# Performance work log

Measured on AMD Instinct MI355X. Metric: run time of the kernel, lower is better.

The kernel has to match this reference:

```python
import jax, jax.numpy as jnp
import numpy as np

B, H, L, N = 128, 1024, 256, 64  # batch, d_model, seq len (l_max), SSM state size


def setup_inputs() -> dict:
    key = jax.random.key(0)
    ks = jax.random.split(key, 8)
    x = jax.random.normal(ks[0], (B, H, L), dtype=jnp.float32)
    # S4D init: dt log-uniform in [1e-3, 1e-1], A = -1/2 + i*pi*n, C ~ N(0,1)
    log_dt = jnp.log(10.0 ** jax.random.uniform(ks[1], (H,), minval=-3.0, maxval=-1.0)).astype(jnp.float32)
    A_real_log = jnp.log(0.5 * jnp.ones((H, N), dtype=jnp.float32))
    A_imag = jnp.tile(jnp.pi * jnp.arange(N, dtype=jnp.float32), (H, 1))
    C_re = jax.random.normal(ks[2], (H, N), dtype=jnp.float32)
    C_im = jax.random.normal(ks[3], (H, N), dtype=jnp.float32)
    D = jax.random.normal(ks[4], (H,), dtype=jnp.float32)
    W_out = (jax.random.normal(ks[5], (2 * H, H), dtype=jnp.float32) / np.sqrt(H)).astype(jnp.float32)
    b_out = jnp.zeros((2 * H,), dtype=jnp.float32)
    return dict(x=x, log_dt=log_dt, A_real_log=A_real_log, A_imag=A_imag,
                C_re=C_re, C_im=C_im, D=D, W_out=W_out, b_out=b_out)


def _s4d_kernel(log_dt, A_real_log, A_imag, C_re, C_im, length):
    """S4D convolution kernel (ZOH discretization), shape (H, length)."""
    dt = jnp.exp(log_dt)[:, None]                      # (H, 1)
    A = -jnp.exp(A_real_log) + 1j * A_imag             # (H, N) complex
    C = C_re + 1j * C_im                               # (H, N)
    dtA = A * dt                                       # (H, N)
    C_disc = C * (jnp.exp(dtA) - 1.0) / A              # ZOH-discretized C
    t = jnp.arange(length, dtype=jnp.float32)
    K = jnp.exp(dtA[:, :, None] * t)                   # (H, N, L) Vandermonde
    return 2.0 * jnp.einsum('hn,hnl->hl', C_disc, K).real


def reference(x, log_dt, A_real_log, A_imag, C_re, C_im, D, W_out, b_out):
    Bq, Hq, Lq = x.shape
    k = _s4d_kernel(log_dt, A_real_log, A_imag, C_re, C_im, Lq)  # (H, L)
    n_fft = 2 * Lq
    k_f = jnp.fft.rfft(k, n=n_fft)                     # (H, L+1)
    x_f = jnp.fft.rfft(x, n=n_fft, axis=-1)            # (B, H, L+1)
    y = jnp.fft.irfft(x_f * k_f[None], n=n_fft, axis=-1)[..., :Lq]
    y = y + D[None, :, None] * x                       # skip connection
    y = jax.nn.gelu(y)                                 # FFTConv activation
    # output linear (d_model -> 2*d_model) + GLU over channel dim
    y = jnp.einsum('bhl,gh->bgl', y, W_out) + b_out[None, :, None]
    a, b = jnp.split(y, 2, axis=1)
    return a * jax.nn.sigmoid(b)                       # (B, H, L)
```

## Files before the change

kernel.cpp:

```cpp
#include <hip/hip_runtime.h>
#include <hip/hip_bf16.h>
#include <cstdint>
#include <cstddef>

typedef __bf16 bf16x8 __attribute__((ext_vector_type(8)));
typedef float  f32x4  __attribute__((ext_vector_type(4)));
typedef unsigned short u16x8 __attribute__((ext_vector_type(8)));

__device__ __forceinline__ unsigned short f2bf(float f) {
    unsigned u = __builtin_bit_cast(unsigned, f);
    u += 0x7fffu + ((u >> 16) & 1u);
    return (unsigned short)(u >> 16);
}
__device__ __forceinline__ float bf2f(unsigned short u) {
    unsigned v = ((unsigned)u) << 16;
    return __builtin_bit_cast(float, v);
}
__device__ __forceinline__ float gelu_tanh(float x) {
    float z = 0.7978845608028654f * (x + 0.044715f * x * x * x);
    float e = __expf(2.0f * z);
    float t = 1.0f - 2.0f / (e + 1.0f);
    return 0.5f * x * (1.0f + t);
}

__global__ void k_build(const float* __restrict__ log_dt,
                        const float* __restrict__ arl,
                        const float* __restrict__ aim,
                        const float* __restrict__ cre,
                        const float* __restrict__ cim,
                        const float* __restrict__ Dp,
                        unsigned short* __restrict__ Tg) {
    __shared__ float sRe[64], sIm[64], sCr[64], sCi[64];
    __shared__ float kk[256];
    const int h = blockIdx.x;
    const int t = threadIdx.x;
    if (t < 64) {
        float dt  = expf(log_dt[h]);
        float ar  = -expf(arl[h * 64 + t]);
        float ai  = aim[h * 64 + t];
        float dre = ar * dt, dim = ai * dt;
        float er  = expf(dre);
        float s, c;
        sincosf(dim, &s, &c);
        float em1r = er * c - 1.0f, em1i = er * s;
        float cr = cre[h * 64 + t], ci = cim[h * 64 + t];
        float pr = cr * em1r - ci * em1i;
        float pi = cr * em1i + ci * em1r;
        float inv = 1.0f / (ar * ar + ai * ai);
        sCr[t] = (pr * ar + pi * ai) * inv;
        sCi[t] = (pi * ar - pr * ai) * inv;
        sRe[t] = dre; sIm[t] = dim;
    }
    __syncthreads();
    float acc = 0.0f;
    const float tf = (float)t;
    #pragma unroll 8
    for (int n = 0; n < 64; n++) {
        float er = expf(sRe[n] * tf);
        float s, c;
        sincosf(sIm[n] * tf, &s, &c);
        acc += sCr[n] * er * c - sCi[n] * er * s;
    }
    kk[t] = 2.0f * acc;
    __syncthreads();
    const float Dh = Dp[h];
    unsigned short* dst = Tg + (size_t)h * 16384;
    for (int c = t; c < 1024; c += 256) {
        const int d = c >> 6, q4 = (c >> 4) & 3, mm = c & 15;
        u16x8 hv, lv;
        #pragma unroll
        for (int e = 0; e < 8; e++) {
            const int idx = 16 * d + mm - (q4 * 8 + e);
            float v = (idx >= 0) ? kk[idx] : 0.0f;
            if (idx == 0) v += Dh;
            unsigned short hb = f2bf(v);
            hv[e] = hb;
            lv[e] = f2bf(v - bf2f(hb));
        }
        *(u16x8*)(dst + c * 8)        = hv;
        *(u16x8*)(dst + 8192 + c * 8) = lv;
    }
}

__global__ __launch_bounds__(256, 2)
void conv_mfma(const float* __restrict__ x,
               const unsigned short* __restrict__ Tg,
               unsigned short* __restrict__ yt2) {
    __shared__ __align__(16) unsigned short smem[32768];
    const int h = blockIdx.x, tid = threadIdx.x;
    const int w = tid >> 6, lane = tid & 63, m = lane & 15, q4 = lane >> 4;

    {
        const unsigned short* tg = Tg + (size_t)h * 16384;
        #pragma unroll
        for (int i = 0; i < 8; i++) {
            int q = i * 256 + tid;
            __builtin_amdgcn_global_load_lds(
                (const __attribute__((address_space(1))) void*)(tg + q * 8),
                (__attribute__((address_space(3))) void*)(smem + q * 8), 16, 0, 0);
        }
    }

    const int sb = tid >> 1, half = tid & 1;
    const float* xrow = x + ((size_t)(sb * 1024 + h) << 8);

    float4 cur[8], nxt[8];
    #pragma unroll
    for (int s = 0; s < 8; s++) cur[s] = *(const float4*)(xrow + half * 32 + s * 4);

    auto STAGE_X = [&](int tile) {
        unsigned short* Xn = smem + 16384 + (tile & 1) * 8192;
        #pragma unroll
        for (int s = 0; s < 8; s++) {
            float4 v = cur[s];
            ushort4 hv, lv;
            hv.x = f2bf(v.x); lv.x = f2bf(v.x - bf2f(hv.x));
            hv.y = f2bf(v.y); lv.y = f2bf(v.y - bf2f(hv.y));
            hv.z = f2bf(v.z); lv.z = f2bf(v.z - bf2f(hv.z));
            hv.w = f2bf(v.w); lv.w = f2bf(v.w - bf2f(hv.w));
            const int base = (((s >> 1) * 128 + sb) << 3) + (s & 1) * 4;
            *(ushort4*)(Xn + base)        = hv;
            *(ushort4*)(Xn + 4096 + base) = lv;
        }
    };

    if (half == 0) STAGE_X(0);

    f32x4 acc[8][4];
    #pragma unroll
    for (int a = 0; a < 8; a++)
        #pragma unroll
        for (int b = 0; b < 4; b++) acc[a][b] = (f32x4){0.f, 0.f, 0.f, 0.f};

    __syncthreads();

    const int fi = (q4 * 16 + m) * 8;

    auto MFMA_BODY = [&](int jt) {
        const unsigned short* Xb = smem + 16384 + (jt & 1) * 8192;
        const int j2 = jt << 1;
        const bool a0 = (w      >= j2);
        const bool a1 = (w + 4  >= j2);
        const bool a2 = (w + 8  >= j2);
        const bool a3 = (w + 12 >= j2);
        bf16x8 th0, tl0, th1, tl1, th2, tl2, th3, tl3;
        if (a0) { int d = w      - j2; th0 = *(const bf16x8*)(smem + d * 512 + fi); tl0 = *(const bf16x8*)(smem + 8192 + d * 512 + fi); }
        if (a1) { int d = w + 4  - j2; th1 = *(const bf16x8*)(smem + d * 512 + fi); tl1 = *(const bf16x8*)(smem + 8192 + d * 512 + fi); }
        if (a2) { int d = w + 8  - j2; th2 = *(const bf16x8*)(smem + d * 512 + fi); tl2 = *(const bf16x8*)(smem + 8192 + d * 512 + fi); }
        if (a3) { int d = w + 12 - j2; th3 = *(const bf16x8*)(smem + d * 512 + fi); tl3 = *(const bf16x8*)(smem + 8192 + d * 512 + fi); }
        #pragma unroll
        for (int fb = 0; fb < 8; fb++) {
            const int xo = (q4 * 128 + fb * 16 + m) * 8;
            bf16x8 xh = *(const bf16x8*)(Xb + xo);
            bf16x8 xl = *(const bf16x8*)(Xb + 4096 + xo);
            if (a0) { acc[fb][0] = __builtin_amdgcn_mfma_f32_16x16x32_bf16(xh, th0, acc[fb][0], 0, 0, 0);
                      acc[fb][0] = __builtin_amdgcn_mfma_f32_16x16x32_bf16(xl, th0, acc[fb][0], 0, 0, 0);
                      acc[fb][0] = __builtin_amdgcn_mfma_f32_16x16x32_bf16(xh, tl0, acc[fb][0], 0, 0, 0); }
            if (a1) { acc[fb][1] = __builtin_amdgcn_mfma_f32_16x16x32_bf16(xh, th1, acc[fb][1], 0, 0, 0);
                      acc[fb][1] = __builtin_amdgcn_mfma_f32_16x16x32_bf16(xl, th1, acc[fb][1], 0, 0, 0);
                      acc[fb][1] = __builtin_amdgcn_mfma_f32_16x16x32_bf16(xh, tl1, acc[fb][1], 0, 0, 0); }
            if (a2) { acc[fb][2] = __builtin_amdgcn_mfma_f32_16x16x32_bf16(xh, th2, acc[fb][2], 0, 0, 0);
                      acc[fb][2] = __builtin_amdgcn_mfma_f32_16x16x32_bf16(xl, th2, acc[fb][2], 0, 0, 0);
                      acc[fb][2] = __builtin_amdgcn_mfma_f32_16x16x32_bf16(xh, tl2, acc[fb][2], 0, 0, 0); }
            if (a3) { acc[fb][3] = __builtin_amdgcn_mfma_f32_16x16x32_bf16(xh, th3, acc[fb][3], 0, 0, 0);
                      acc[fb][3] = __builtin_amdgcn_mfma_f32_16x16x32_bf16(xl, th3, acc[fb][3], 0, 0, 0);
                      acc[fb][3] = __builtin_amdgcn_mfma_f32_16x16x32_bf16(xh, tl3, acc[fb][3], 0, 0, 0); }
        }
    };

    #pragma unroll 1
    for (int g = 0; g < 4; g++) {
        if (g < 3) {
            #pragma unroll
            for (int s = 0; s < 8; s++)
                nxt[s] = *(const float4*)(xrow + (g + 1) * 64 + half * 32 + s * 4);
        }
        MFMA_BODY(2 * g);
        if (half == 1) STAGE_X(2 * g + 1);
        __syncthreads();
        MFMA_BODY(2 * g + 1);
        if (g < 3) {
            #pragma unroll
            for (int s = 0; s < 8; s++) cur[s] = nxt[s];
            if (half == 0) STAGE_X(2 * g + 2);
        }
        __syncthreads();
    }

    const size_t ybase = (size_t)h * 32768;
    #pragma unroll
    for (int p = 0; p < 2; p++) {
        #pragma unroll
        for (int tt = 0; tt < 2; tt++) {
            const int ti = p * 2 + tt;
            const int lr = (w + 4 * ti) * 16 + m - p * 128;
            #pragma unroll
            for (int fb = 0; fb < 8; fb++) {
                #pragma unroll
                for (int rg = 0; rg < 4; rg++) {
                    const int b = fb * 16 + q4 * 4 + rg;
                    smem[b * 136 + lr] = f2bf(gelu_tanh(acc[fb][ti][rg]));
                }
            }
        }
        __syncthreads();
        #pragma unroll
        for (int bb = 0; bb < 4; bb++) {
            const int bp = bb * 32 + (tid >> 3);
            #pragma unroll
            for (int s = 0; s < 2; s++) {
                const int chk = (tid & 7) + 8 * s;
                u16x8 v = *(const u16x8*)(smem + bp * 136 + chk * 8);
                *(u16x8*)(yt2 + ybase + (size_t)bp * 256 + p * 128 + chk * 8) = v;
            }
        }
        __syncthreads();
    }
}

__global__ void transp(const unsigned short* __restrict__ yt2,
                       unsigned short* __restrict__ yt) {
    __shared__ __align__(16) unsigned short tl[32768];
    const int tid = threadIdx.x;
    const int m0 = blockIdx.x * 256, h0 = blockIdx.y * 128;
    #pragma unroll
    for (int i = 0; i < 16; i++) {
        const int q = i * 256 + tid;
        const int hh = q >> 5, c = q & 31;
        u16x8 v = *(const u16x8*)(yt2 + (size_t)(h0 + hh) * 32768 + m0 + c * 8);
        const int pc = c ^ (hh & 31);
        *(u16x8*)(tl + hh * 256 + pc * 8) = v;
    }
    __syncthreads();
    #pragma unroll
    for (int i = 0; i < 16; i++) {
        const int q = i * 256 + tid;
        const int mm = q >> 4, hc = q & 15;
        u16x8 o;
        #pragma unroll
        for (int e = 0; e < 8; e++) {
            const int hh = hc * 8 + e;
            const int pm = ((mm >> 3) ^ (hh & 31)) * 8 + (mm & 7);
            o[e] = tl[hh * 256 + pm];
        }
        *(u16x8*)(yt + (size_t)(m0 + mm) * 1024 + h0 + hc * 8) = o;
    }
}

__global__ void pack_w2(const float* __restrict__ W, unsigned short* __restrict__ Wp) {
    const int p   = blockIdx.x;
    const int g32 = p >> 5, r32 = p & 31;
    const int g   = (r32 < 16) ? (g32 * 16 + r32) : (1024 + g32 * 16 + (r32 - 16));
    const int t   = threadIdx.x;
    const float4 v = *(const float4*)(W + (size_t)g * 1024 + t * 4);
    ushort4 o;
    o.x = f2bf(v.x); o.y = f2bf(v.y); o.z = f2bf(v.z); o.w = f2bf(v.w);
    *(ushort4*)(Wp + (size_t)p * 1024 + t * 4) = o;
}

__global__ __launch_bounds__(512, 2)
void gemm_glu2(const unsigned short* __restrict__ yt,
               const unsigned short* __restrict__ Wp,
               const float* __restrict__ bo,
               float* __restrict__ out) {
    __shared__ __align__(16) unsigned short smem[65536];
    const int tid = threadIdx.x;
    const int bid = (int)blockIdx.x;
    const int b1  = (bid & 7) * 128 + (bid >> 3);
    const int bm  = b1 >> 3;
    const int bn_ = b1 & 7;
    const int wid = tid >> 6, lane = tid & 63;
    const int m = lane & 15, q4 = lane >> 4;
    const int wm = wid >> 2, wn = wid & 3;

    const size_t abase = (size_t)bm * 256 * 1024;
    const size_t bbase = (size_t)bn_ * 256 * 1024;

    f32x4 acc[8][4];
    #pragma unroll
    for (int fr = 0; fr < 8; fr++)
        #pragma unroll
        for (int fc = 0; fc < 4; fc++) acc[fr][fc] = (f32x4){0.f, 0.f, 0.f, 0.f};

    auto STAGE = [&](int t) {
        const int bufo = (t & 1) << 15;
        const int k0 = t * 64;
        #pragma unroll
        for (int i = 0; i < 4; i++) {
            int q = i * 512 + tid;
            int r = q >> 3, c = (q & 7) ^ (r & 7);
            const unsigned short* gp = yt + abase + (size_t)r * 1024 + k0 + c * 8;
            __builtin_amdgcn_global_load_lds(
                (const __attribute__((address_space(1))) void*)gp,
                (__attribute__((address_space(3))) void*)(smem + bufo + q * 8), 16, 0, 0);
        }
        #pragma unroll
        for (int i = 0; i < 4; i++) {
            int q = i * 512 + tid;
            int r = q >> 3, c = (q & 7) ^ (r & 7);
            const unsigned short* gp = Wp + bbase + (size_t)r * 1024 + k0 + c * 8;
            __builtin_amdgcn_global_load_lds(
                (const __attribute__((address_space(1))) void*)gp,
                (__attribute__((address_space(3))) void*)(smem + bufo + 16384 + q * 8), 16, 0, 0);
        }
    };

    STAGE(0);
    STAGE(1);
    asm volatile("s_waitcnt vmcnt(8)" ::: "memory");
    __builtin_amdgcn_s_barrier();

    const int arow0 = wm * 128;
    const int brow0 = wn * 64;

    for (int t = 0; t < 16; t++) {
        const int bufo = (t & 1) << 15;
        bf16x8 af[8][2], bf[4][2];
        #pragma unroll
        for (int fr = 0; fr < 8; fr++) {
            const int r = arow0 + fr * 16 + m;
            #pragma unroll
            for (int ks = 0; ks < 2; ks++) {
                const int c = (ks * 4 + q4) ^ (r & 7);
                af[fr][ks] = *(const bf16x8*)(smem + bufo + r * 64 + c * 8);
            }
        }
        #pragma unroll
        for (int fc = 0; fc < 4; fc++) {
            const int r = brow0 + fc * 16 + m;
            #pragma unroll
            for (int ks = 0; ks < 2; ks++) {
                const int c = (ks * 4 + q4) ^ (r & 7);
                bf[fc][ks] = *(const bf16x8*)(smem + bufo + 16384 + r * 64 + c * 8);
            }
        }
        asm volatile("s_waitcnt lgkmcnt(0)" ::: "memory");
        __builtin_amdgcn_sched_barrier(0);
        __builtin_amdgcn_s_barrier();
        if (t < 14) STAGE(t + 2);
        __builtin_amdgcn_s_setprio(1);
        #pragma unroll
        for (int ks = 0; ks < 2; ks++)
            #pragma unroll
            for (int fr = 0; fr < 8; fr++)
                #pragma unroll
                for (int fc = 0; fc < 4; fc++)
                    acc[fr][fc] = __builtin_amdgcn_mfma_f32_16x16x32_bf16(
                        af[fr][ks], bf[fc][ks], acc[fr][fc], 0, 0, 0);
        __builtin_amdgcn_s_setprio(0);
        if (t < 14) asm volatile("s_waitcnt vmcnt(8)" ::: "memory");
        else        asm volatile("s_waitcnt vmcnt(0)" ::: "memory");
        __builtin_amdgcn_s_barrier();
    }

    const size_t outb = ((size_t)bm) << 18;
    const int lbase = wm * 128;
    #pragma unroll
    for (int fcp = 0; fcp < 2; fcp++) {
        const int go = (bn_ * 8 + wn * 2 + fcp) * 16 + m;
        const float boa = bo[go], bog = bo[1024 + go];
        #pragma unroll
        for (int fr = 0; fr < 8; fr++) {
            f32x4 av = acc[fr][2 * fcp];
            f32x4 gv = acc[fr][2 * fcp + 1];
            f32x4 o;
            #pragma unroll
            for (int rg = 0; rg < 4; rg++) {
                float a = av[rg] + boa, g = gv[rg] + bog;
                o[rg] = a / (1.0f + __expf(-g));
            }
            const int l = lbase + fr * 16 + q4 * 4;
            *(f32x4*)(out + outb + (((size_t)go) << 8) + l) = o;
        }
    }
}

extern "C" void kernel_launch(void* const* d_in, const int* in_sizes, int n_in,
                              void* d_out, int out_size, void* d_ws, size_t ws_size,
                              hipStream_t stream) {
    const float* x   = (const float*)d_in[0];
    const float* ldt = (const float*)d_in[1];
    const float* arl = (const float*)d_in[2];
    const float* aim = (const float*)d_in[3];
    const float* cre = (const float*)d_in[4];
    const float* cim = (const float*)d_in[5];
    const float* D   = (const float*)d_in[6];
    const float* Wo  = (const float*)d_in[7];
    const float* bo  = (const float*)d_in[8];
    float* out = (float*)d_out;

    const size_t MB = (size_t)1 << 20;
    const size_t need = 132 * MB;
    if (ws_size < need) return;

    unsigned short* Wp  = (unsigned short*)d_ws;
    unsigned short* Tg  = (unsigned short*)((char*)d_ws + 4 * MB);
    unsigned short* yt  = (unsigned short*)((char*)d_ws + 4 * MB);
    unsigned short* yt2 = (unsigned short*)((char*)d_ws + 68 * MB);

    k_build  <<<1024, 256, 0, stream>>>(ldt, arl, aim, cre, cim, D, Tg);
    pack_w2  <<<2048, 256, 0, stream>>>(Wo, Wp);
    conv_mfma<<<1024, 256, 0, stream>>>(x, Tg, yt2);
    transp   <<<dim3(128, 8), 256, 0, stream>>>(yt2, yt);
    gemm_glu2<<<1024, 512, 0, stream>>>(yt, Wp, bo, out);
}
```

Before: 460.7 us.

## Restructure conv MFMA loop with load-balanced tiles and larger staged x blocks

The conv kernel now stages four x tiles (half the sequence) at once into a larger shared buffer with XOR swizzling, and computes in two phases instead of eight double-buffered steps. Output tiles are assigned per wave in a balanced pattern (w, 7-w, 8+w, 15-w) so the causal triangular work is spread evenly and masked MFMAs are skipped via loop bounds. Raising shared memory use and relaxing launch bounds to one block lowers occupancy, and the overlap of global loads with compute is lost. Minor changes are sincospif in the kernel build and padded rows in the transpose buffer to reduce bank conflicts.

```diff
diff --git a/kernel.cpp b/kernel.cpp
--- a/kernel.cpp
+++ b/kernel.cpp
@@ -30,7 +30,7 @@
                         const float* __restrict__ cim,
                         const float* __restrict__ Dp,
                         unsigned short* __restrict__ Tg) {
-    __shared__ float sRe[64], sIm[64], sCr[64], sCi[64];
+    __shared__ float sRe[64], sW[64], sCr[64], sCi[64];
     __shared__ float kk[256];
     const int h = blockIdx.x;
     const int t = threadIdx.x;
@@ -49,7 +49,8 @@
         float inv = 1.0f / (ar * ar + ai * ai);
         sCr[t] = (pr * ar + pi * ai) * inv;
         sCi[t] = (pi * ar - pr * ai) * inv;
-        sRe[t] = dre; sIm[t] = dim;
+        sRe[t] = dre;
+        sW[t]  = dim * 0.31830988618379067f;
     }
     __syncthreads();
     float acc = 0.0f;
@@ -58,7 +59,7 @@
     for (int n = 0; n < 64; n++) {
         float er = expf(sRe[n] * tf);
         float s, c;
-        sincosf(sIm[n] * tf, &s, &c);
+        sincospif(sW[n] * tf, &s, &c);
         acc += sCr[n] * er * c - sCi[n] * er * s;
     }
     kk[t] = 2.0f * acc;
@@ -82,11 +83,11 @@
     }
 }
 
-__global__ __launch_bounds__(256, 2)
+__global__ __launch_bounds__(256, 1)
 void conv_mfma(const float* __restrict__ x,
                const unsigned short* __restrict__ Tg,
                unsigned short* __restrict__ yt2) {
-    __shared__ __align__(16) unsigned short smem[32768];
+    __shared__ __align__(16) unsigned short smem[49152];
     const int h = blockIdx.x, tid = threadIdx.x;
     const int w = tid >> 6, lane = tid & 63, m = lane & 15, q4 = lane >> 4;
 
@@ -101,105 +102,85 @@
         }
     }
 
-    const int sb = tid >> 1, half = tid & 1;
-    const float* xrow = x + ((size_t)(sb * 1024 + h) << 8);
-
-    float4 cur[8], nxt[8];
-    #pragma unroll
-    for (int s = 0; s < 8; s++) cur[s] = *(const float4*)(xrow + half * 32 + s * 4);
-
-    auto STAGE_X = [&](int tile) {
-        unsigned short* Xn = smem + 16384 + (tile & 1) * 8192;
-        #pragma unroll
-        for (int s = 0; s < 8; s++) {
-            float4 v = cur[s];
-            ushort4 hv, lv;
-            hv.x = f2bf(v.x); lv.x = f2bf(v.x - bf2f(hv.x));
-            hv.y = f2bf(v.y); lv.y = f2bf(v.y - bf2f(hv.y));
-            hv.z = f2bf(v.z); lv.z = f2bf(v.z - bf2f(hv.z));
-            hv.w = f2bf(v.w); lv.w = f2bf(v.w - bf2f(hv.w));
-            const int base = (((s >> 1) * 128 + sb) << 3) + (s & 1) * 4;
-            *(ushort4*)(Xn + base)        = hv;
-            *(ushort4*)(Xn + 4096 + base) = lv;
+    auto STAGE_X = [&](int P) {
+        #pragma unroll
+        for (int jj = 0; jj < 4; jj++) {
+            const int jt = P * 4 + jj;
+            #pragma unroll
+            for (int i = 0; i < 4; i++) {
+                const int slot = i * 256 + tid;
+                const int b = slot >> 3, j4 = slot & 7;
+                float4 v = *(const float4*)(x + (((size_t)(b * 1024 + h)) << 8) + jt * 32 + j4 * 4);
+                ushort4 hv, lv;
+                hv.x = f2bf(v.x); lv.x = f2bf(v.x - bf2f(hv.x));
+                hv.y = f2bf(v.y); lv.y = f2bf(v.y - bf2f(hv.y));
+                hv.z = f2bf(v.z); lv.z = f2bf(v.z - bf2f(hv.z));
+                hv.w = f2bf(v.w); lv.w = f2bf(v.w - bf2f(hv.w));
+                const int q4s = j4 >> 1, off = (j4 & 1) * 4;
+                const int base = 16384 + jj * 4096 + (q4s * 128 + (b ^ q4s)) * 8 + off;
+                *(ushort4*)(smem + base)         = hv;
+                *(ushort4*)(smem + 16384 + base) = lv;
+            }
         }
     };
 
-    if (half == 0) STAGE_X(0);
-
     f32x4 acc[8][4];
     #pragma unroll
     for (int a = 0; a < 8; a++)
         #pragma unroll
         for (int b = 0; b < 4; b++) acc[a][b] = (f32x4){0.f, 0.f, 0.f, 0.f};
 
-    __syncthreads();
-
     const int fi = (q4 * 16 + m) * 8;
-
-    auto MFMA_BODY = [&](int jt) {
-        const unsigned short* Xb = smem + 16384 + (jt & 1) * 8192;
-        const int j2 = jt << 1;
-        const bool a0 = (w      >= j2);
-        const bool a1 = (w + 4  >= j2);
-        const bool a2 = (w + 8  >= j2);
-        const bool a3 = (w + 12 >= j2);
-        bf16x8 th0, tl0, th1, tl1, th2, tl2, th3, tl3;
-        if (a0) { int d = w      - j2; th0 = *(const bf16x8*)(smem + d * 512 + fi); tl0 = *(const bf16x8*)(smem + 8192 + d * 512 + fi); }
-        if (a1) { int d = w + 4  - j2; th1 = *(const bf16x8*)(smem + d * 512 + fi); tl1 = *(const bf16x8*)(smem + 8192 + d * 512 + fi); }
-        if (a2) { int d = w + 8  - j2; th2 = *(const bf16x8*)(smem + d * 512 + fi); tl2 = *(const bf16x8*)(smem + 8192 + d * 512 + fi); }
-        if (a3) { int d = w + 12 - j2; th3 = *(const bf16x8*)(smem + d * 512 + fi); tl3 = *(const bf16x8*)(smem + 8192 + d * 512 + fi); }
-        #pragma unroll
-        for (int fb = 0; fb < 8; fb++) {
-            const int xo = (q4 * 128 + fb * 16 + m) * 8;
-            bf16x8 xh = *(const bf16x8*)(Xb + xo);
-            bf16x8 xl = *(const bf16x8*)(Xb + 4096 + xo);
-            if (a0) { acc[fb][0] = __builtin_amdgcn_mfma_f32_16x16x32_bf16(xh, th0, acc[fb][0], 0, 0, 0);
-                      acc[fb][0] = __builtin_amdgcn_mfma_f32_16x16x32_bf16(xl, th0, acc[fb][0], 0, 0, 0);
-                      acc[fb][0] = __builtin_amdgcn_mfma_f32_16x16x32_bf16(xh, tl0, acc[fb][0], 0, 0, 0); }
-            if (a1) { acc[fb][1] = __builtin_amdgcn_mfma_f32_16x16x32_bf16(xh, th1, acc[fb][1], 0, 0, 0);
-                      acc[fb][1] = __builtin_amdgcn_mfma_f32_16x16x32_bf16(xl, th1, acc[fb][1], 0, 0, 0);
-                      acc[fb][1] = __builtin_amdgcn_mfma_f32_16x16x32_bf16(xh, tl1, acc[fb][1], 0, 0, 0); }
-            if (a2) { acc[fb][2] = __builtin_amdgcn_mfma_f32_16x16x32_bf16(xh, th2, acc[fb][2], 0, 0, 0);
-                      acc[fb][2] = __builtin_amdgcn_mfma_f32_16x16x32_bf16(xl, th2, acc[fb][2], 0, 0, 0);
-                      acc[fb][2] = __builtin_amdgcn_mfma_f32_16x16x32_bf16(xh, tl2, acc[fb][2], 0, 0, 0); }
-            if (a3) { acc[fb][3] = __builtin_amdgcn_mfma_f32_16x16x32_bf16(xh, th3, acc[fb][3], 0, 0, 0);
-                      acc[fb][3] = __builtin_amdgcn_mfma_f32_16x16x32_bf16(xl, th3, acc[fb][3], 0, 0, 0);
-                      acc[fb][3] = __builtin_amdgcn_mfma_f32_16x16x32_bf16(xh, tl3, acc[fb][3], 0, 0, 0); }
+    const int tiles[4] = { w, 7 - w, 8 + w, 15 - w };
+
+    auto COMPUTE = [&](int P) {
+        #pragma unroll
+        for (int s = 0; s < 4; s++) {
+            const int ti = tiles[s];
+            const int jmax = ti >> 1;
+            const int jhi = (jmax < P * 4 + 3) ? jmax : (P * 4 + 3);
+            for (int jt = P * 4; jt <= jhi; jt++) {
+                const int d = ti - 2 * jt;
+                bf16x8 th  = *(const bf16x8*)(smem + d * 512 + fi);
+                bf16x8 tlo = *(const bf16x8*)(smem + 8192 + d * 512 + fi);
+                const int xb = 16384 + (jt & 3) * 4096;
+                #pragma unroll
+                for (int fb = 0; fb < 8; fb++) {
+                    const int xo = (q4 * 128 + ((fb * 16 + m) ^ q4)) * 8;
+                    bf16x8 xh = *(const bf16x8*)(smem + xb + xo);
+                    bf16x8 xl = *(const bf16x8*)(smem + 16384 + xb + xo);
+                    acc[fb][s] = __builtin_amdgcn_mfma_f32_16x16x32_bf16(xh, th,  acc[fb][s], 0, 0, 0);
+                    acc[fb][s] = __builtin_amdgcn_mfma_f32_16x16x32_bf16(xl, th,  acc[fb][s], 0, 0, 0);
+                    acc[fb][s] = __builtin_amdgcn_mfma_f32_16x16x32_bf16(xh, tlo, acc[fb][s], 0, 0, 0);
+                }
+            }
         }
     };
 
-    #pragma unroll 1
-    for (int g = 0; g < 4; g++) {
-        if (g < 3) {
-            #pragma unroll
-            for (int s = 0; s < 8; s++)
-                nxt[s] = *(const float4*)(xrow + (g + 1) * 64 + half * 32 + s * 4);
-        }
-        MFMA_BODY(2 * g);
-        if (half == 1) STAGE_X(2 * g + 1);
-        __syncthreads();
-        MFMA_BODY(2 * g + 1);
-        if (g < 3) {
-            #pragma unroll
-            for (int s = 0; s < 8; s++) cur[s] = nxt[s];
-            if (half == 0) STAGE_X(2 * g + 2);
-        }
-        __syncthreads();
-    }
+    STAGE_X(0);
+    __syncthreads();
+    COMPUTE(0);
+    __syncthreads();
+    STAGE_X(1);
+    __syncthreads();
+    COMPUTE(1);
+    __syncthreads();
 
     const size_t ybase = (size_t)h * 32768;
     #pragma unroll
     for (int p = 0; p < 2; p++) {
         #pragma unroll
         for (int tt = 0; tt < 2; tt++) {
-            const int ti = p * 2 + tt;
-            const int lr = (w + 4 * ti) * 16 + m - p * 128;
+            const int s = p * 2 + tt;
+            const int L = (tt == 0) ? (p == 0 ? w : 8 + w)
+                                    : (p == 0 ? 7 - w : 15 - w);
+            const int lr = L * 16 + m - p * 128;
             #pragma unroll
             for (int fb = 0; fb < 8; fb++) {
                 #pragma unroll
                 for (int rg = 0; rg < 4; rg++) {
                     const int b = fb * 16 + q4 * 4 + rg;
-                    smem[b * 136 + lr] = f2bf(gelu_tanh(acc[fb][ti][rg]));
+                    smem[b * 136 + lr] = f2bf(gelu_tanh(acc[fb][s][rg]));
                 }
             }
         }
@@ -208,8 +189,8 @@
         for (int bb = 0; bb < 4; bb++) {
             const int bp = bb * 32 + (tid >> 3);
             #pragma unroll
-            for (int s = 0; s < 2; s++) {
-                const int chk = (tid & 7) + 8 * s;
+            for (int s2 = 0; s2 < 2; s2++) {
+                const int chk = (tid & 7) + 8 * s2;
                 u16x8 v = *(const u16x8*)(smem + bp * 136 + chk * 8);
                 *(u16x8*)(yt2 + ybase + (size_t)bp * 256 + p * 128 + chk * 8) = v;
             }
@@ -220,7 +201,7 @@
 
 __global__ void transp(const unsigned short* __restrict__ yt2,
                        unsigned short* __restrict__ yt) {
-    __shared__ __align__(16) unsigned short tl[32768];
+    __shared__ __align__(16) unsigned short tl[128 * 264];
     const int tid = threadIdx.x;
     const int m0 = blockIdx.x * 256, h0 = blockIdx.y * 128;
     #pragma unroll
@@ -228,8 +209,7 @@
         const int q = i * 256 + tid;
         const int hh = q >> 5, c = q & 31;
         u16x8 v = *(const u16x8*)(yt2 + (size_t)(h0 + hh) * 32768 + m0 + c * 8);
-        const int pc = c ^ (hh & 31);
-        *(u16x8*)(tl + hh * 256 + pc * 8) = v;
+        *(u16x8*)(tl + hh * 264 + ((c ^ (hh & 31)) << 3)) = v;
     }
     __syncthreads();
     #pragma unroll
@@ -240,8 +220,7 @@
         #pragma unroll
         for (int e = 0; e < 8; e++) {
             const int hh = hc * 8 + e;
-            const int pm = ((mm >> 3) ^ (hh & 31)) * 8 + (mm & 7);
-            o[e] = tl[hh * 256 + pm];
+            o[e] = tl[hh * 264 + (((mm >> 3) ^ (hh & 31)) << 3) + (mm & 7)];
         }
         *(u16x8*)(yt + (size_t)(m0 + mm) * 1024 + h0 + hc * 8) = o;
     }
```

Measured after the change: 492.8 us. 7.0% more time.
